# Optimization experiments

Measured on AMD Instinct MI355X. Metric: run time of the kernel, lower is better.

The kernel has to match this reference:

```python
import jax, jax.numpy as jnp
import numpy as np

NC = 2            # num_classes
CONF_THR = 0.7
IOU_THR = 0.2

_PI, _PJ = np.triu_indices(9, k=1)   # 36 candidate edge directions for min-area rect


def _decode_level(out, stride):
    # out: [C,h,w]; scale (x,y) channels by stride and add the pixel grid, flatten to [h*w, C]
    C, h, w = out.shape
    gw = (stride * jnp.arange(w, dtype=out.dtype))[None, :]
    gh = (stride * jnp.arange(h, dtype=out.dtype))[:, None]
    out = out.at[NC + 1].set(out[NC + 1] * stride + gw)
    out = out.at[NC + 2].set(out[NC + 2] * stride + gh)
    return out.reshape(C, -1).T


def _min_area_polygons(pts18):
    # pts18: (N,18) interleaved (a,b) coordinate pairs of 9 points.
    # Min-area enclosing rectangle: optimal rect is aligned with some point-pair direction;
    # brute-force all 36 pairs (superset of hull edges) -> exact result, fully vectorized.
    P = pts18.reshape(-1, 9, 2)                       # (N,9,2)
    d = P[:, _PJ] - P[:, _PI]                         # (N,36,2)
    nrm = jnp.sqrt(jnp.sum(d * d, -1) + 1e-12)
    c, s = d[..., 0] / nrm, d[..., 1] / nrm           # (N,36)
    a, b = P[..., 0][:, None, :], P[..., 1][:, None, :]   # (N,1,9)
    u = a * c[..., None] + b * s[..., None]           # rotate by -theta
    v = -a * s[..., None] + b * c[..., None]
    umin, umax = u.min(-1), u.max(-1)
    vmin, vmax = v.min(-1), v.max(-1)
    area = (umax - umin) * (vmax - vmin)              # (N,36)
    k = jnp.argmin(area, 1)[:, None]
    tk = lambda z: jnp.take_along_axis(z, k, 1)[:, 0]
    c, s, umin, umax, vmin, vmax = map(tk, (c, s, umin, umax, vmin, vmax))
    cu = jnp.stack([umin, umax, umax, umin], -1)      # rect corners in rotated frame
    cv = jnp.stack([vmin, vmin, vmax, vmax], -1)
    ca = cu * c[:, None] - cv * s[:, None]            # rotate back
    cb = cu * s[:, None] + cv * c[:, None]
    return jnp.stack([ca, cb], -1).reshape(-1, 8)     # (N,8) interleaved corners


def _points_in_quad(pts, quad):
    # pts (M,2), quad (4,2) convex with consistent winding -> (M,) bool
    e = jnp.roll(quad, -1, 0) - quad
    r = pts[:, None, :] - quad[None]
    cr = e[None, :, 0] * r[..., 1] - e[None, :, 1] * r[..., 0]
    return (cr >= 0).all(-1) | (cr <= 0).all(-1)


def _box_decoder(rect):
    # rect (N,8) -> (N,5) [cx, cy, w, h, angle]; y_first=True convention from the source
    w = jnp.sqrt((rect[:, 0] - rect[:, 2]) ** 2 + (rect[:, 1] - rect[:, 3]) ** 2)
    h = jnp.sqrt((rect[:, 4] - rect[:, 2]) ** 2 + (rect[:, 5] - rect[:, 3]) ** 2)
    cx = rect[:, 1:8:2].sum(1) * 0.25
    cy = rect[:, 0:8:2].sum(1) * 0.25
    ang = jnp.arctan((rect[:, 0] - rect[:, 2]) / (rect[:, 1] - rect[:, 3]))
    return jnp.stack([cx, cy, w, h, ang], -1)


def _rbox_corners(b):
    cx, cy, w, h, a = b[0], b[1], b[2], b[3], b[4]
    cs, sn = jnp.cos(a), jnp.sin(a)
    lx = jnp.array([-0.5, 0.5, 0.5, -0.5]) * w
    ly = jnp.array([-0.5, -0.5, 0.5, 0.5]) * h
    return jnp.stack([cx + lx * cs - ly * sn, cy + lx * sn + ly * cs], -1)  # (4,2)


def _quad_inter_area(A, B):
    # exact intersection area of two convex quads A,B (4,2):
    # candidates = corners of each inside the other + all 16 edge-edge intersections,
    # sorted by angle around their centroid, masked shoelace.
    inA = _points_in_quad(B, A)
    inB = _points_in_quad(A, B)
    rA = jnp.roll(A, -1, 0) - A
    rB = jnp.roll(B, -1, 0) - B
    qp = B[None] - A[:, None]                                  # (4,4,2)
    den = rA[:, None, 0] * rB[None, :, 1] - rA[:, None, 1] * rB[None, :, 0]
    dsafe = jnp.where(jnp.abs(den) < 1e-9, 1e-9, den)
    t = (qp[..., 0] * rB[None, :, 1] - qp[..., 1] * rB[None, :, 0]) / dsafe
    uu = (qp[..., 0] * rA[:, None, 1] - qp[..., 1] * rA[:, None, 0]) / dsafe
    okx = (jnp.abs(den) > 1e-9) & (t >= 0) & (t <= 1) & (uu >= 0) & (uu <= 1)
    X = A[:, None] + t[..., None] * rA[:, None]
    pts = jnp.concatenate([A, B, X.reshape(16, 2)], 0)          # (24,2)
    val = jnp.concatenate([inB, inA, okx.reshape(16)], 0)
    n = val.sum()
    cen = jnp.sum(jnp.where(val[:, None], pts, 0.0), 0) / jnp.maximum(n, 1)
    rel = pts - cen
    ang = jnp.where(val, jnp.arctan2(rel[:, 1], rel[:, 0]), 1e9)
    o = jnp.argsort(ang)
    rp, vs = rel[o], val[o]
    rp = jnp.where(vs[:, None], rp, rp[0])   # invalid slots -> first valid vertex (zero-area edges)
    nx = jnp.roll(rp, -1, 0)
    area = 0.5 * jnp.abs(jnp.sum(rp[:, 0] * nx[:, 1] - rp[:, 1] * nx[:, 0]))
    return jnp.where(n >= 3, area, 0.0)


def _forward(out3, out4, out5, off1_l3, off1_l4, off1_l5, offf_l3, offf_l4, offf_l5):
    outs = jnp.concatenate([_decode_level(out3[0], 4),
                            _decode_level(out4[0], 8),
                            _decode_level(out5[0], 16)], 0)          # (N, NC+3)
    flat = lambda z: z[0].reshape(18, -1).T
    off1 = jnp.concatenate([flat(off1_l3), flat(off1_l4), flat(off1_l5)], 0)
    offf = jnp.concatenate([flat(offf_l3), flat(offf_l4), flat(offf_l5)], 0) + off1
    N = outs.shape[0]
    x, y = outs[:, NC + 1], outs[:, NC + 2]
    offf = offf + jnp.tile(jnp.stack([y, x], -1), (1, 9))            # (y,x) interleaved, 9 points
    xs, ys = offf[:, 1:18:2], offf[:, 0:18:2]
    area = (xs.max(1) - xs.min(1)) * (ys.max(1) - ys.min(1)) / 40.0
    conf = outs[:, 0]
    conf_mask = conf > CONF_THR * jax.nn.sigmoid(area)
    rect = _min_area_polygons(offf)                                  # (N,8)
    boxes5 = _box_decoder(rect)                                      # (N,5)
    corners = jax.vmap(_rbox_corners)(boxes5)                        # (N,4,2)
    areas5 = boxes5[:, 2] * boxes5[:, 3]
    position = outs[:, NC + 1:]                                      # (N,2) = (x,y)
    pts_yx = jnp.stack([position[:, 1], position[:, 0]], -1)         # (y,x), matches rect plane
    quads = rect.reshape(N, 4, 2)
    order = jnp.argsort(jnp.where(conf_mask, conf, -jnp.inf))[::-1]

    def step(carry, i):
        suppressed, keep = carry
        active = jnp.logical_not(suppressed[i])
        keep = keep.at[i].set(active)
        inside = _points_in_quad(pts_yx, quads[i])                   # points_in_polygons
        inter = jax.vmap(lambda C: _quad_inter_area(corners[i], C))(corners)
        iou = inter / (areas5[i] + areas5 - inter + 1e-9)            # box_iou_rotated
        suppressed = suppressed | (active & (inside | (iou >= IOU_THR)))
        return (suppressed, keep), None

    init = (jnp.logical_not(conf_mask), jnp.zeros(N, dtype=bool))
    (_, keep), _ = jax.lax.scan(step, init, order)

    cls = outs[:, 1:NC + 1]
    maxc = cls.max(1)
    masks = jnp.stack([keep & (cls[:, i] == maxc) for i in range(NC)], 0)  # (NC,N)
    cnt = masks.sum(1)
    result = jnp.where(masks[:, :, None], position[None], 0.0)             # (NC,N,2) padded
    rect_out = rect * keep[:, None].astype(rect.dtype)                     # (N,8) padded
    return cnt, result, rect_out


def setup_inputs() -> dict:
    key = jax.random.key(0)
    shapes = [("out3", (1, NC + 3, 32, 32)), ("out4", (1, NC + 3, 16, 16)), ("out5", (1, NC + 3, 8, 8)),
              ("off1_l3", (1, 18, 32, 32)), ("off1_l4", (1, 18, 16, 16)), ("off1_l5", (1, 18, 8, 8)),
              ("offf_l3", (1, 18, 32, 32)), ("offf_l4", (1, 18, 16, 16)), ("offf_l5", (1, 18, 8, 8))]
    ks = jax.random.split(key, len(shapes))
    return {n: jax.random.normal(k, s, dtype=jnp.float32) for (n, s), k in zip(shapes, ks)}


def reference(out3, out4, out5, off1_l3, off1_l4, off1_l5, offf_l3, offf_l4, offf_l5):
    return _forward(out3, out4, out5, off1_l3, off1_l4, off1_l5, offf_l3, offf_l4, offf_l5)
```

## Files before the change

kernel.cpp:

```cpp
#include <hip/hip_runtime.h>
#include <math.h>

#define N_DET 1344
#define NW 21
#define MW_MAX 8
#define T2S 9
#define PAIR_CAP 40000


__device__ __forceinline__ bool pt_in_quad4(const float* qx, const float* qy,
                                            float px, float py) {
    bool allp = true, alln = true;
#pragma unroll
    for (int k = 0; k < 4; k++) {
        int k1 = (k + 1) & 3;
        float ex = qx[k1] - qx[k], ey = qy[k1] - qy[k];
        float rx = px - qx[k],     ry = py - qy[k];
        float cr = ex * ry - ey * rx;
        allp = allp && (cr >= 0.f);
        alln = alln && (cr <= 0.f);
    }
    return allp || alln;
}

__device__ float quad_inter_area(const float* Ax, const float* Ay,
                                 const float* Bx, const float* By) {
    float px[24], py[24];
    unsigned vmask = 0;
    int n = 0;
#pragma unroll
    for (int k = 0; k < 4; k++) {
        px[k] = Ax[k]; py[k] = Ay[k];
        if (pt_in_quad4(Bx, By, Ax[k], Ay[k])) { vmask |= 1u << k; n++; }
    }
#pragma unroll
    for (int k = 0; k < 4; k++) {
        px[4 + k] = Bx[k]; py[4 + k] = By[k];
        if (pt_in_quad4(Ax, Ay, Bx[k], By[k])) { vmask |= 1u << (4 + k); n++; }
    }
#pragma unroll
    for (int k = 0; k < 4; k++) {
        int k1 = (k + 1) & 3;
        float rax = Ax[k1] - Ax[k], ray = Ay[k1] - Ay[k];
#pragma unroll
        for (int l = 0; l < 4; l++) {
            int l1 = (l + 1) & 3;
            float rbx = Bx[l1] - Bx[l], rby = By[l1] - By[l];
            float qpx = Bx[l] - Ax[k],  qpy = By[l] - Ay[k];
            float den = rax * rby - ray * rbx;
            float ad  = fabsf(den);
            float dsafe = (ad < 1e-9f) ? 1e-9f : den;
            float t = (qpx * rby - qpy * rbx) / dsafe;
            float u = (qpx * ray - qpy * rax) / dsafe;
            bool ok = (ad > 1e-9f) && t >= 0.f && t <= 1.f && u >= 0.f && u <= 1.f;
            int id = 8 + k * 4 + l;
            px[id] = Ax[k] + t * rax;
            py[id] = Ay[k] + t * ray;
            if (ok) { vmask |= 1u << id; n++; }
        }
    }
    float cx = 0.f, cy = 0.f;
#pragma unroll
    for (int m = 0; m < 24; m++)
        if ((vmask >> m) & 1u) { cx += px[m]; cy += py[m]; }
    int mx = (n < 1) ? 1 : n;
    cx = cx / (float)mx;
    cy = cy / (float)mx;

    unsigned long long key[32];
    float sx[32], sy[32];
#pragma unroll
    for (int m = 0; m < 24; m++) {
        float rx = px[m] - cx, ry = py[m] - cy;
        float a = ((vmask >> m) & 1u) ? atan2f(ry, rx) : 1e9f;
        unsigned u = __float_as_uint(a);
        u = (u & 0x80000000u) ? ~u : (u | 0x80000000u);
        key[m] = (((unsigned long long)u) << 6) | (unsigned)m;
        sx[m] = rx; sy[m] = ry;
    }
#pragma unroll
    for (int m = 24; m < 32; m++) { key[m] = ~0ull; sx[m] = 0.f; sy[m] = 0.f; }

#pragma unroll
    for (int k = 2; k <= 32; k <<= 1) {
#pragma unroll
        for (int j = k >> 1; j > 0; j >>= 1) {
#pragma unroll
            for (int t = 0; t < 32; t++) {
                int l = t ^ j;
                if (l > t) {
                    bool up = ((t & k) == 0);
                    bool sw = up ? (key[t] > key[l]) : (key[t] < key[l]);
                    if (sw) {
                        unsigned long long tk = key[t]; key[t] = key[l]; key[l] = tk;
                        float tx = sx[t]; sx[t] = sx[l]; sx[l] = tx;
                        float ty = sy[t]; sy[t] = sy[l]; sy[l] = ty;
                    }
                }
            }
        }
    }

    unsigned ut = __float_as_uint(1e9f) | 0x80000000u;
    unsigned long long kt = ((unsigned long long)ut) << 6;
    float fx = sx[0], fy = sy[0];
    float qx2[24], qy2[24];
#pragma unroll
    for (int m = 0; m < 24; m++) {
        bool v = key[m] < kt;
        qx2[m] = v ? sx[m] : fx;
        qy2[m] = v ? sy[m] : fy;
    }
    float ssum = 0.f;
#pragma unroll
    for (int m = 0; m < 24; m++) {
        int m1 = (m + 1) % 24;
        ssum += qx2[m] * qy2[m1] - qy2[m] * qx2[m1];
    }
    float area = 0.5f * fabsf(ssum);
    return (n >= 3) ? area : 0.f;
}

__device__ bool iou_suppress(const float* __restrict__ cor, const float* __restrict__ a5,
                             int i, int j) {
    float Axr[4], Ayr[4], Bxr[4], Byr[4];
#pragma unroll
    for (int k = 0; k < 4; k++) {
        Axr[k] = cor[i * 8 + 2 * k]; Ayr[k] = cor[i * 8 + 2 * k + 1];
        Bxr[k] = cor[j * 8 + 2 * k]; Byr[k] = cor[j * 8 + 2 * k + 1];
    }
    float inter = quad_inter_area(Axr, Ayr, Bxr, Byr);
    float iou = inter / (a5[i] + a5[j] - inter + 1e-9f);
    return iou >= 0.2f;
}

__global__ void k_decode(const float* __restrict__ out3, const float* __restrict__ out4,
                         const float* __restrict__ out5,
                         const float* __restrict__ o1l3, const float* __restrict__ o1l4,
                         const float* __restrict__ o1l5,
                         const float* __restrict__ ofl3, const float* __restrict__ ofl4,
                         const float* __restrict__ ofl5,
                         float* conf, float* cls0, float* cls1, float* xx, float* yy,
                         float* a5, float* ccx, float* ccy, float* rr,
                         float* rect, float* cor, int* mask, int* Mcnt, int* pairCnt) {
    int n = blockIdx.x * blockDim.x + threadIdx.x;
    if (n >= N_DET) return;
    if (n == 0) { *Mcnt = 0; *pairCnt = 0; }
    const float *out, *o1, *of;
    int w, idx; float stride;
    if (n < 1024)      { out = out3; o1 = o1l3; of = ofl3; w = 32; idx = n;        stride = 4.f; }
    else if (n < 1280) { out = out4; o1 = o1l4; of = ofl4; w = 16; idx = n - 1024; stride = 8.f; }
    else               { out = out5; o1 = o1l5; of = ofl5; w = 8;  idx = n - 1280; stride = 16.f; }
    int hw = w * w;
    int row = idx / w, col = idx % w;
    float cf = out[0 * hw + idx];
    float c0 = out[1 * hw + idx];
    float c1 = out[2 * hw + idx];
    float x  = out[3 * hw + idx] * stride + stride * (float)col;
    float y  = out[4 * hw + idx] * stride + stride * (float)row;

    float Pa[9], Pb[9];
    float minb = INFINITY, maxb = -INFINITY, mina = INFINITY, maxa = -INFINITY;
#pragma unroll
    for (int k = 0; k < 9; k++) {
        float a = of[(2 * k) * hw + idx]     + o1[(2 * k) * hw + idx]     + y;
        float b = of[(2 * k + 1) * hw + idx] + o1[(2 * k + 1) * hw + idx] + x;
        Pa[k] = a; Pb[k] = b;
        mina = fminf(mina, a); maxa = fmaxf(maxa, a);
        minb = fminf(minb, b); maxb = fmaxf(maxb, b);
    }
    float area = (maxb - minb) * (maxa - mina) / 40.0f;
    float sg = 1.0f / (1.0f + expf(-area));
    int m = (cf > 0.7f * sg) ? 1 : 0;

    float best = INFINITY, bc = 0.f, bs = 0.f;
    float bumin = 0.f, bumax = 0.f, bvmin = 0.f, bvmax = 0.f;
#pragma unroll
    for (int i = 0; i < 9; i++) {
#pragma unroll
        for (int j = i + 1; j < 9; j++) {
            float d0 = Pa[j] - Pa[i], d1 = Pb[j] - Pb[i];
            float nr = sqrtf(d0 * d0 + d1 * d1 + 1e-12f);
            float c = d0 / nr, s = d1 / nr;
            float umin = INFINITY, umax = -INFINITY, vmin = INFINITY, vmax = -INFINITY;
#pragma unroll
            for (int k = 0; k < 9; k++) {
                float u =  Pa[k] * c + Pb[k] * s;
                float v = -Pa[k] * s + Pb[k] * c;
                umin = fminf(umin, u); umax = fmaxf(umax, u);
                vmin = fminf(vmin, v); vmax = fmaxf(vmax, v);
            }
            float ar = (umax - umin) * (vmax - vmin);
            if (ar < best) { best = ar; bc = c; bs = s;
                             bumin = umin; bumax = umax; bvmin = vmin; bvmax = vmax; }
        }
    }
    float cu[4] = {bumin, bumax, bumax, bumin};
    float cv[4] = {bvmin, bvmin, bvmax, bvmax};
    float r8[8];
#pragma unroll
    for (int k = 0; k < 4; k++) {
        r8[2 * k]     = cu[k] * bc - cv[k] * bs;
        r8[2 * k + 1] = cu[k] * bs + cv[k] * bc;
    }
    float w5 = sqrtf((r8[0] - r8[2]) * (r8[0] - r8[2]) + (r8[1] - r8[3]) * (r8[1] - r8[3]));
    float h5 = sqrtf((r8[4] - r8[2]) * (r8[4] - r8[2]) + (r8[5] - r8[3]) * (r8[5] - r8[3]));
    float cx = (r8[1] + r8[3] + r8[5] + r8[7]) * 0.25f;
    float cy = (r8[0] + r8[2] + r8[4] + r8[6]) * 0.25f;
    float ang = atanf((r8[0] - r8[2]) / (r8[1] - r8[3]));
    float cs = cosf(ang), sn = sinf(ang);
    const float lxs[4] = {-0.5f, 0.5f, 0.5f, -0.5f};
    const float lys[4] = {-0.5f, -0.5f, 0.5f, 0.5f};
#pragma unroll
    for (int k = 0; k < 4; k++) {
        cor[n * 8 + 2 * k]     = cx + lxs[k] * w5 * cs - lys[k] * h5 * sn;
        cor[n * 8 + 2 * k + 1] = cy + lxs[k] * w5 * sn + lys[k] * h5 * cs;
    }
#pragma unroll
    for (int k = 0; k < 8; k++) rect[n * 8 + k] = r8[k];
    conf[n] = cf; cls0[n] = c0; cls1[n] = c1;
    xx[n] = x; yy[n] = y; a5[n] = w5 * h5; mask[n] = m;
    ccx[n] = cx; ccy[n] = cy;
    rr[n] = 0.5f * sqrtf(w5 * w5 + h5 * h5);
}

__global__ __launch_bounds__(64) void k_order(const float* __restrict__ conf,
                                              const int* __restrict__ mask,
                                              int* order, int* Mcnt) {
    int b = blockIdx.x;
    int lane = threadIdx.x;
    int mb = mask[b];
    float ki = mb ? conf[b] : -INFINITY;
    int rank = 0;
    for (int j = lane; j < N_DET; j += 64) {
        float kj = mask[j] ? conf[j] : -INFINITY;
        rank += ((kj > ki) || (kj == ki && j > b)) ? 1 : 0;
    }
    for (int off = 32; off; off >>= 1) rank += __shfl_down(rank, off, 64);
    if (lane == 0) {
        order[rank] = b;
        if (mb) atomicAdd(Mcnt, 1);
    }
}

__global__ __launch_bounds__(256) void k_pairs_a(
        const float* __restrict__ rect, const float* __restrict__ cor,
        const float* __restrict__ a5,
        const float* __restrict__ xx, const float* __restrict__ yy,
        const float* __restrict__ ccx, const float* __restrict__ ccy,
        const float* __restrict__ rr,
        const int* __restrict__ order, const int* __restrict__ Mcnt,
        unsigned long long* __restrict__ S2, unsigned int* __restrict__ pairs,
        int* __restrict__ pairCnt) {
    int M = *Mcnt;
    if (M <= 0) return;
    int MW = (M + 63) >> 6;
    bool use_list = (MW <= MW_MAX);
    int lane  = threadIdx.x & 63;
    int gwave = (blockIdx.x * 256 + threadIdx.x) >> 6;
    int nwave = (gridDim.x * 256) >> 6;
    int total = M * MW;
    for (int t = gwave; t < total; t += nwave) {
        int p = t / MW;
        int w = t - p * MW;
        int i = order[p];
        int q = w * 64 + lane;
        bool valid = q < M;
        int j = valid ? order[q] : i;

        float cbi = ccx[i], cai = ccy[i], ri = rr[i];
        float da = yy[j] - cai, db = xx[j] - cbi;
        float rin = ri + 0.1f;
        bool inside = false;
        if (da * da + db * db <= rin * rin) {
            float qxr[4], qyr[4];
#pragma unroll
            for (int k = 0; k < 4; k++) { qxr[k] = rect[i * 8 + 2 * k]; qyr[k] = rect[i * 8 + 2 * k + 1]; }
            inside = pt_in_quad4(qxr, qyr, yy[j], xx[j]);
        }
        bool bit = valid && inside;
        unsigned long long bb = __ballot(bit);
        if (lane == 0) S2[p * MW + w] = bb;

        float ex = cbi - ccx[j], ey = cai - ccy[j];
        float rs = ri + rr[j] + 0.1f;
        bool iou_pos = valid && (q != p) && !bit && (ex * ex + ey * ey <= rs * rs);
        if (use_list) {
            unsigned long long pm = __ballot(iou_pos);
            if (pm) {
                int cw = __popcll(pm);
                int base = 0;
                if (lane == 0) base = atomicAdd(pairCnt, cw);
                base = __shfl(base, 0, 64);
                if (iou_pos) {
                    int pos = base + __popcll(pm & ((1ull << lane) - 1ull));
                    if (pos < PAIR_CAP) {
                        pairs[pos] = ((unsigned)p << 11) | (unsigned)q;
                    } else if (iou_suppress(cor, a5, i, j)) {
                        atomicOr(&S2[p * MW + w], 1ull << (q & 63));
                    }
                }
            }
        } else if (iou_pos) {
            if (iou_suppress(cor, a5, i, j))
                atomicOr(&S2[p * MW + w], 1ull << (q & 63));
        }
    }
}

__global__ __launch_bounds__(256) void k_pairs_b(
        const float* __restrict__ cor, const float* __restrict__ a5,
        const int* __restrict__ order, const int* __restrict__ Mcnt,
        const int* __restrict__ pairCnt, const unsigned int* __restrict__ pairs,
        unsigned long long* __restrict__ S2) {
    int M = *Mcnt;
    int MW = (M + 63) >> 6;
    if (MW > MW_MAX) return;
    int cnt = *pairCnt; if (cnt > PAIR_CAP) cnt = PAIR_CAP;
    int stride = gridDim.x * 256;
    for (int t = blockIdx.x * 256 + threadIdx.x; t < cnt; t += stride) {
        unsigned v = pairs[t];
        int p = (int)(v >> 11), q = (int)(v & 2047u);
        int i = order[p], j = order[q];
        if (iou_suppress(cor, a5, i, j))
            atomicOr(&S2[p * MW + (q >> 6)], 1ull << (q & 63));
    }
}

__global__ __launch_bounds__(512) void k_scan_out(
    const float* __restrict__ cls0, const float* __restrict__ cls1,
    const float* __restrict__ xx, const float* __restrict__ yy,
    const float* __restrict__ rect,
    const int* __restrict__ order, const int* __restrict__ Mcnt,
    const unsigned long long* __restrict__ S2, float* __restrict__ out) {
    __shared__ int order_s[N_DET];
    __shared__ unsigned long long T2[512 * T2S];
    __shared__ unsigned long long Kfin[MW_MAX];
    __shared__ unsigned int keep32[(N_DET + 31) / 32];
    __shared__ int cnt_s[2];
    int tid = threadIdx.x;
    int lane = tid & 63, wid = tid >> 6;
    int M = *Mcnt;
    int MW = (M + 63) >> 6;
    for (int t = tid; t < N_DET; t += 512) order_s[t] = order[t];
    for (int t = tid; t < (N_DET + 31) / 32; t += 512) keep32[t] = 0u;
    if (tid < 2) cnt_s[tid] = 0;
    if (tid < MW_MAX) Kfin[tid] = 0ull;
    __syncthreads();

    if (M > 0 && MW <= MW_MAX) {
        for (int blk = wid; blk < MW * MW; blk += 8) {
            int wp = blk / MW, wq = blk - wp * MW;
            int pp = wp * 64 + lane;
            unsigned long long x = (pp < M) ? S2[pp * MW + wq] : 0ull;
#pragma unroll
            for (int b = 0; b < 64; b++) {
                unsigned long long bb = __ballot((x >> b) & 1ull);
                if (lane == b) T2[(wq * 64 + b) * T2S + wp] = bb;
            }
        }
        __syncthreads();

        if (wid == 0) {
            unsigned long long kw[MW_MAX];
#pragma unroll
            for (int w = 0; w < MW_MAX; w++) {
                int lo = w * 64;
                kw[w] = (M > lo) ? ((M - lo >= 64) ? ~0ull : ((1ull << (M - lo)) - 1ull)) : 0ull;
            }
            unsigned long long pmask = lane ? ((1ull << lane) - 1ull) : 0ull;
            for (int it = 0; it <= M; ++it) {
                bool changed = false;
#pragma unroll
                for (int k = 0; k < MW_MAX; k++) {
                    if (k < MW) {
                        int q = k * 64 + lane;
                        const unsigned long long* row = &T2[q * T2S];
                        unsigned long long sup = 0ull;
#pragma unroll
                        for (int w = 0; w < MW_MAX; w++) {
                            if (w < k)       sup |= row[w] & kw[w];
                            else if (w == k) sup |= row[w] & kw[w] & pmask;
                        }
                        bool nb = (q < M) && (sup == 0ull);
                        unsigned long long nw = __ballot(nb);
                        changed |= (nw != kw[k]);
                        kw[k] = nw;
                    }
                }
                if (!changed) break;
            }
            if (lane == 0) {
#pragma unroll
                for (int w = 0; w < MW_MAX; w++) Kfin[w] = kw[w];
            }
        }
        __syncthreads();
        for (int t = tid; t < M; t += 512) {
            if ((Kfin[t >> 6] >> (t & 63)) & 1ull) {
                int i = order_s[t];
                atomicOr(&keep32[i >> 5], 1u << (i & 31));
            }
        }
    } else if (M > 0) {
        if (wid == 0) {
            unsigned long long rem = 0ull;
            int lo = lane * 64;
            if (M > lo) rem = (M - lo >= 64) ? ~0ull : ((1ull << (M - lo)) - 1ull);
            for (int guard = 0; guard < N_DET; guard++) {
                unsigned long long vote = __ballot(rem != 0ull);
                if (!vote) break;
                int w = __builtin_ctzll(vote);
                unsigned long long wd = __shfl(rem, w, 64);
                int b = __builtin_ctzll(wd);
                int p = w * 64 + b;
                int i = order_s[p];
                if (lane == 0) atomicOr(&keep32[i >> 5], 1u << (i & 31));
                unsigned long long rowv = (lane < MW) ? S2[p * MW + lane] : 0ull;
                rem &= ~rowv;
                if (lane == w) rem &= ~(1ull << b);
            }
        }
    }
    __syncthreads();

    int c0 = 0, c1 = 0;
    for (int n = tid; n < N_DET; n += 512) {
        bool kp = (keep32[n >> 5] >> (n & 31)) & 1u;
        float a = cls0[n], b = cls1[n];
        float mxc = fmaxf(a, b);
        bool m0 = kp && (a == mxc);
        bool m1 = kp && (b == mxc);
        float x = xx[n], y = yy[n];
        out[2 + 0 * N_DET * 2 + n * 2 + 0] = m0 ? x : 0.f;
        out[2 + 0 * N_DET * 2 + n * 2 + 1] = m0 ? y : 0.f;
        out[2 + 1 * N_DET * 2 + n * 2 + 0] = m1 ? x : 0.f;
        out[2 + 1 * N_DET * 2 + n * 2 + 1] = m1 ? y : 0.f;
        float kf = kp ? 1.f : 0.f;
#pragma unroll
        for (int k = 0; k < 8; k++)
            out[2 + 2 * N_DET * 2 + n * 8 + k] = rect[n * 8 + k] * kf;
        c0 += m0 ? 1 : 0;
        c1 += m1 ? 1 : 0;
    }
    if (c0) atomicAdd(&cnt_s[0], c0);
    if (c1) atomicAdd(&cnt_s[1], c1);
    __syncthreads();
    if (tid == 0) { out[0] = (float)cnt_s[0]; out[1] = (float)cnt_s[1]; }
}

extern "C" void kernel_launch(void* const* d_in, const int* in_sizes, int n_in,
                              void* d_out, int out_size, void* d_ws, size_t ws_size,
                              hipStream_t stream) {
    const float* out3 = (const float*)d_in[0];
    const float* out4 = (const float*)d_in[1];
    const float* out5 = (const float*)d_in[2];
    const float* o1l3 = (const float*)d_in[3];
    const float* o1l4 = (const float*)d_in[4];
    const float* o1l5 = (const float*)d_in[5];
    const float* ofl3 = (const float*)d_in[6];
    const float* ofl4 = (const float*)d_in[7];
    const float* ofl5 = (const float*)d_in[8];
    float* out = (float*)d_out;

    const int N = N_DET;
    float* wsf  = (float*)d_ws;
    float* conf = wsf + 0 * N;
    float* cls0 = wsf + 1 * N;
    float* cls1 = wsf + 2 * N;
    float* xx   = wsf + 3 * N;
    float* yy   = wsf + 4 * N;
    float* a5   = wsf + 5 * N;
    float* ccx  = wsf + 6 * N;
    float* ccy  = wsf + 7 * N;
    float* rr   = wsf + 8 * N;
    float* rect = wsf + 9 * N;
    float* cor  = wsf + 17 * N;
    int* mask   = (int*)(wsf + 25 * N);
    int* order  = mask + N;
    int* Mcnt   = order + N;
    int* pairCnt = Mcnt + 1;
    unsigned long long* S2 = (unsigned long long*)(wsf + 27 * N + 4);
    unsigned int* pairs = (unsigned int*)((char*)S2 + 32768);

    k_decode<<<(N + 255) / 256, 256, 0, stream>>>(out3, out4, out5, o1l3, o1l4, o1l5,
                                                  ofl3, ofl4, ofl5,
                                                  conf, cls0, cls1, xx, yy, a5,
                                                  ccx, ccy, rr, rect, cor, mask, Mcnt, pairCnt);
    k_order<<<N, 64, 0, stream>>>(conf, mask, order, Mcnt);
    k_pairs_a<<<1024, 256, 0, stream>>>(rect, cor, a5, xx, yy, ccx, ccy, rr,
                                        order, Mcnt, S2, pairs, pairCnt);
    k_pairs_b<<<64, 256, 0, stream>>>(cor, a5, order, Mcnt, pairCnt, pairs, S2);
    k_scan_out<<<1, 512, 0, stream>>>(cls0, cls1, xx, yy, rect, order, Mcnt, S2, out);
}
```

Baseline: 142.9 us.

## Fuse NMS pipeline into single cooperative kernel with grid-wide syncs

Replaces five separate kernel launches (decode, ordering, pair test, pair IoU, scan/output) with one cooperative kernel of 256 blocks that uses grid.sync between phases. The mask count moves from an atomic to per-wave ballot counts, and the bitmask transpose is spread across the grid instead of running in one block. This targets launch and inter-kernel gaps in a latency-bound pipeline, at the cost of grid barriers and fewer waves for the ordering and pair phases. The pair-list capacity is also raised.

```diff
diff --git a/kernel.cpp b/kernel.cpp
--- a/kernel.cpp
+++ b/kernel.cpp
@@ -1,11 +1,13 @@
 #include <hip/hip_runtime.h>
+#include <hip/hip_cooperative_groups.h>
 #include <math.h>
 
 #define N_DET 1344
-#define NW 21
 #define MW_MAX 8
 #define T2S 9
-#define PAIR_CAP 40000
+#define PAIR_CAP 200000
+
+namespace cg = cooperative_groups;
 
 
 __device__ __forceinline__ bool pt_in_quad4(const float* qx, const float* qy,
@@ -134,234 +136,220 @@
     return iou >= 0.2f;
 }
 
-__global__ void k_decode(const float* __restrict__ out3, const float* __restrict__ out4,
-                         const float* __restrict__ out5,
-                         const float* __restrict__ o1l3, const float* __restrict__ o1l4,
-                         const float* __restrict__ o1l5,
-                         const float* __restrict__ ofl3, const float* __restrict__ ofl4,
-                         const float* __restrict__ ofl5,
-                         float* conf, float* cls0, float* cls1, float* xx, float* yy,
-                         float* a5, float* ccx, float* ccy, float* rr,
-                         float* rect, float* cor, int* mask, int* Mcnt, int* pairCnt) {
-    int n = blockIdx.x * blockDim.x + threadIdx.x;
-    if (n >= N_DET) return;
-    if (n == 0) { *Mcnt = 0; *pairCnt = 0; }
-    const float *out, *o1, *of;
-    int w, idx; float stride;
-    if (n < 1024)      { out = out3; o1 = o1l3; of = ofl3; w = 32; idx = n;        stride = 4.f; }
-    else if (n < 1280) { out = out4; o1 = o1l4; of = ofl4; w = 16; idx = n - 1024; stride = 8.f; }
-    else               { out = out5; o1 = o1l5; of = ofl5; w = 8;  idx = n - 1280; stride = 16.f; }
-    int hw = w * w;
-    int row = idx / w, col = idx % w;
-    float cf = out[0 * hw + idx];
-    float c0 = out[1 * hw + idx];
-    float c1 = out[2 * hw + idx];
-    float x  = out[3 * hw + idx] * stride + stride * (float)col;
-    float y  = out[4 * hw + idx] * stride + stride * (float)row;
-
-    float Pa[9], Pb[9];
-    float minb = INFINITY, maxb = -INFINITY, mina = INFINITY, maxa = -INFINITY;
-#pragma unroll
-    for (int k = 0; k < 9; k++) {
-        float a = of[(2 * k) * hw + idx]     + o1[(2 * k) * hw + idx]     + y;
-        float b = of[(2 * k + 1) * hw + idx] + o1[(2 * k + 1) * hw + idx] + x;
-        Pa[k] = a; Pb[k] = b;
-        mina = fminf(mina, a); maxa = fmaxf(maxa, a);
-        minb = fminf(minb, b); maxb = fmaxf(maxb, b);
-    }
-    float area = (maxb - minb) * (maxa - mina) / 40.0f;
-    float sg = 1.0f / (1.0f + expf(-area));
-    int m = (cf > 0.7f * sg) ? 1 : 0;
-
-    float best = INFINITY, bc = 0.f, bs = 0.f;
-    float bumin = 0.f, bumax = 0.f, bvmin = 0.f, bvmax = 0.f;
-#pragma unroll
-    for (int i = 0; i < 9; i++) {
-#pragma unroll
-        for (int j = i + 1; j < 9; j++) {
-            float d0 = Pa[j] - Pa[i], d1 = Pb[j] - Pb[i];
-            float nr = sqrtf(d0 * d0 + d1 * d1 + 1e-12f);
-            float c = d0 / nr, s = d1 / nr;
-            float umin = INFINITY, umax = -INFINITY, vmin = INFINITY, vmax = -INFINITY;
-#pragma unroll
-            for (int k = 0; k < 9; k++) {
-                float u =  Pa[k] * c + Pb[k] * s;
-                float v = -Pa[k] * s + Pb[k] * c;
-                umin = fminf(umin, u); umax = fmaxf(umax, u);
-                vmin = fminf(vmin, v); vmax = fmaxf(vmax, v);
-            }
-            float ar = (umax - umin) * (vmax - vmin);
-            if (ar < best) { best = ar; bc = c; bs = s;
-                             bumin = umin; bumax = umax; bvmin = vmin; bvmax = vmax; }
-        }
-    }
-    float cu[4] = {bumin, bumax, bumax, bumin};
-    float cv[4] = {bvmin, bvmin, bvmax, bvmax};
-    float r8[8];
-#pragma unroll
-    for (int k = 0; k < 4; k++) {
-        r8[2 * k]     = cu[k] * bc - cv[k] * bs;
-        r8[2 * k + 1] = cu[k] * bs + cv[k] * bc;
-    }
-    float w5 = sqrtf((r8[0] - r8[2]) * (r8[0] - r8[2]) + (r8[1] - r8[3]) * (r8[1] - r8[3]));
-    float h5 = sqrtf((r8[4] - r8[2]) * (r8[4] - r8[2]) + (r8[5] - r8[3]) * (r8[5] - r8[3]));
-    float cx = (r8[1] + r8[3] + r8[5] + r8[7]) * 0.25f;
-    float cy = (r8[0] + r8[2] + r8[4] + r8[6]) * 0.25f;
-    float ang = atanf((r8[0] - r8[2]) / (r8[1] - r8[3]));
-    float cs = cosf(ang), sn = sinf(ang);
-    const float lxs[4] = {-0.5f, 0.5f, 0.5f, -0.5f};
-    const float lys[4] = {-0.5f, -0.5f, 0.5f, 0.5f};
-#pragma unroll
-    for (int k = 0; k < 4; k++) {
-        cor[n * 8 + 2 * k]     = cx + lxs[k] * w5 * cs - lys[k] * h5 * sn;
-        cor[n * 8 + 2 * k + 1] = cy + lxs[k] * w5 * sn + lys[k] * h5 * cs;
-    }
-#pragma unroll
-    for (int k = 0; k < 8; k++) rect[n * 8 + k] = r8[k];
-    conf[n] = cf; cls0[n] = c0; cls1[n] = c1;
-    xx[n] = x; yy[n] = y; a5[n] = w5 * h5; mask[n] = m;
-    ccx[n] = cx; ccy[n] = cy;
-    rr[n] = 0.5f * sqrtf(w5 * w5 + h5 * h5);
-}
-
-__global__ __launch_bounds__(64) void k_order(const float* __restrict__ conf,
-                                              const int* __restrict__ mask,
-                                              int* order, int* Mcnt) {
-    int b = blockIdx.x;
-    int lane = threadIdx.x;
-    int mb = mask[b];
-    float ki = mb ? conf[b] : -INFINITY;
-    int rank = 0;
-    for (int j = lane; j < N_DET; j += 64) {
-        float kj = mask[j] ? conf[j] : -INFINITY;
-        rank += ((kj > ki) || (kj == ki && j > b)) ? 1 : 0;
-    }
-    for (int off = 32; off; off >>= 1) rank += __shfl_down(rank, off, 64);
-    if (lane == 0) {
-        order[rank] = b;
-        if (mb) atomicAdd(Mcnt, 1);
-    }
-}
-
-__global__ __launch_bounds__(256) void k_pairs_a(
-        const float* __restrict__ rect, const float* __restrict__ cor,
-        const float* __restrict__ a5,
-        const float* __restrict__ xx, const float* __restrict__ yy,
-        const float* __restrict__ ccx, const float* __restrict__ ccy,
-        const float* __restrict__ rr,
-        const int* __restrict__ order, const int* __restrict__ Mcnt,
-        unsigned long long* __restrict__ S2, unsigned int* __restrict__ pairs,
-        int* __restrict__ pairCnt) {
-    int M = *Mcnt;
-    if (M <= 0) return;
+struct KArgs {
+    const float *out3, *out4, *out5, *o1l3, *o1l4, *o1l5, *ofl3, *ofl4, *ofl5;
+    float *keyArr, *cls0, *cls1, *xx, *yy, *a5, *ccx, *ccy, *rr, *rect, *cor;
+    int *order, *mcount_w, *pairCnt;
+    unsigned long long *S2, *T2g;
+    unsigned int *pairs;
+    float *out;
+};
+
+__global__ __launch_bounds__(256) void k_all(KArgs a) {
+    cg::grid_group grid = cg::this_grid();
+    const int tid  = threadIdx.x;
+    const int bid  = blockIdx.x;
+    const int lane = tid & 63;
+    const int wib  = tid >> 6;
+    const int gwave = bid * 4 + wib;
+
+    if (bid < 21 && wib == 0) {
+        int n = bid * 64 + lane;
+        const float *out, *o1, *of;
+        int w, idx; float stride;
+        if (n < 1024)      { out = a.out3; o1 = a.o1l3; of = a.ofl3; w = 32; idx = n;        stride = 4.f; }
+        else if (n < 1280) { out = a.out4; o1 = a.o1l4; of = a.ofl4; w = 16; idx = n - 1024; stride = 8.f; }
+        else               { out = a.out5; o1 = a.o1l5; of = a.ofl5; w = 8;  idx = n - 1280; stride = 16.f; }
+        int hw = w * w;
+        int row = idx / w, col = idx % w;
+        float cf = out[0 * hw + idx];
+        float c0 = out[1 * hw + idx];
+        float c1 = out[2 * hw + idx];
+        float x  = out[3 * hw + idx] * stride + stride * (float)col;
+        float y  = out[4 * hw + idx] * stride + stride * (float)row;
+
+        float Pa[9], Pb[9];
+        float minb = INFINITY, maxb = -INFINITY, mina = INFINITY, maxa = -INFINITY;
+#pragma unroll
+        for (int k = 0; k < 9; k++) {
+            float aa = of[(2 * k) * hw + idx]     + o1[(2 * k) * hw + idx]     + y;
+            float bb = of[(2 * k + 1) * hw + idx] + o1[(2 * k + 1) * hw + idx] + x;
+            Pa[k] = aa; Pb[k] = bb;
+            mina = fminf(mina, aa); maxa = fmaxf(maxa, aa);
+            minb = fminf(minb, bb); maxb = fmaxf(maxb, bb);
+        }
+        float area = (maxb - minb) * (maxa - mina) / 40.0f;
+        float sg = 1.0f / (1.0f + expf(-area));
+        int m = (cf > 0.7f * sg) ? 1 : 0;
+
+        float best = INFINITY, bc = 0.f, bs = 0.f;
+        float bumin = 0.f, bumax = 0.f, bvmin = 0.f, bvmax = 0.f;
+#pragma unroll
+        for (int i = 0; i < 9; i++) {
+#pragma unroll
+            for (int j = i + 1; j < 9; j++) {
+                float d0 = Pa[j] - Pa[i], d1 = Pb[j] - Pb[i];
+                float nr = sqrtf(d0 * d0 + d1 * d1 + 1e-12f);
+                float c = d0 / nr, s = d1 / nr;
+                float umin = INFINITY, umax = -INFINITY, vmin = INFINITY, vmax = -INFINITY;
+#pragma unroll
+                for (int k = 0; k < 9; k++) {
+                    float u =  Pa[k] * c + Pb[k] * s;
+                    float v = -Pa[k] * s + Pb[k] * c;
+                    umin = fminf(umin, u); umax = fmaxf(umax, u);
+                    vmin = fminf(vmin, v); vmax = fmaxf(vmax, v);
+                }
+                float ar = (umax - umin) * (vmax - vmin);
+                if (ar < best) { best = ar; bc = c; bs = s;
+                                 bumin = umin; bumax = umax; bvmin = vmin; bvmax = vmax; }
+            }
+        }
+        float cu[4] = {bumin, bumax, bumax, bumin};
+        float cv[4] = {bvmin, bvmin, bvmax, bvmax};
+        float r8[8];
+#pragma unroll
+        for (int k = 0; k < 4; k++) {
+            r8[2 * k]     = cu[k] * bc - cv[k] * bs;
+            r8[2 * k + 1] = cu[k] * bs + cv[k] * bc;
+        }
+        float w5 = sqrtf((r8[0] - r8[2]) * (r8[0] - r8[2]) + (r8[1] - r8[3]) * (r8[1] - r8[3]));
+        float h5 = sqrtf((r8[4] - r8[2]) * (r8[4] - r8[2]) + (r8[5] - r8[3]) * (r8[5] - r8[3]));
+        float cx = (r8[1] + r8[3] + r8[5] + r8[7]) * 0.25f;
+        float cy = (r8[0] + r8[2] + r8[4] + r8[6]) * 0.25f;
+        float ang = atanf((r8[0] - r8[2]) / (r8[1] - r8[3]));
+        float cs = cosf(ang), sn = sinf(ang);
+        const float lxs[4] = {-0.5f, 0.5f, 0.5f, -0.5f};
+        const float lys[4] = {-0.5f, -0.5f, 0.5f, 0.5f};
+#pragma unroll
+        for (int k = 0; k < 4; k++) {
+            a.cor[n * 8 + 2 * k]     = cx + lxs[k] * w5 * cs - lys[k] * h5 * sn;
+            a.cor[n * 8 + 2 * k + 1] = cy + lxs[k] * w5 * sn + lys[k] * h5 * cs;
+        }
+#pragma unroll
+        for (int k = 0; k < 8; k++) a.rect[n * 8 + k] = r8[k];
+        a.keyArr[n] = m ? cf : -INFINITY;
+        a.cls0[n] = c0; a.cls1[n] = c1;
+        a.xx[n] = x; a.yy[n] = y; a.a5[n] = w5 * h5;
+        a.ccx[n] = cx; a.ccy[n] = cy;
+        a.rr[n] = 0.5f * sqrtf(w5 * w5 + h5 * h5);
+        unsigned long long mb = __ballot(m != 0);
+        if (lane == 0) a.mcount_w[bid] = (int)__popcll(mb);
+    }
+    if (bid == 21 && tid == 0) *a.pairCnt = 0;
+    grid.sync();
+
+    int M = 0;
+#pragma unroll
+    for (int k = 0; k < 21; k++) M += a.mcount_w[k];
     int MW = (M + 63) >> 6;
-    bool use_list = (MW <= MW_MAX);
-    int lane  = threadIdx.x & 63;
-    int gwave = (blockIdx.x * 256 + threadIdx.x) >> 6;
-    int nwave = (gridDim.x * 256) >> 6;
-    int total = M * MW;
-    for (int t = gwave; t < total; t += nwave) {
-        int p = t / MW;
-        int w = t - p * MW;
-        int i = order[p];
-        int q = w * 64 + lane;
-        bool valid = q < M;
-        int j = valid ? order[q] : i;
-
-        float cbi = ccx[i], cai = ccy[i], ri = rr[i];
-        float da = yy[j] - cai, db = xx[j] - cbi;
-        float rin = ri + 0.1f;
-        bool inside = false;
-        if (da * da + db * db <= rin * rin) {
-            float qxr[4], qyr[4];
-#pragma unroll
-            for (int k = 0; k < 4; k++) { qxr[k] = rect[i * 8 + 2 * k]; qyr[k] = rect[i * 8 + 2 * k + 1]; }
-            inside = pt_in_quad4(qxr, qyr, yy[j], xx[j]);
-        }
-        bool bit = valid && inside;
-        unsigned long long bb = __ballot(bit);
-        if (lane == 0) S2[p * MW + w] = bb;
-
-        float ex = cbi - ccx[j], ey = cai - ccy[j];
-        float rs = ri + rr[j] + 0.1f;
-        bool iou_pos = valid && (q != p) && !bit && (ex * ex + ey * ey <= rs * rs);
-        if (use_list) {
-            unsigned long long pm = __ballot(iou_pos);
-            if (pm) {
-                int cw = __popcll(pm);
-                int base = 0;
-                if (lane == 0) base = atomicAdd(pairCnt, cw);
-                base = __shfl(base, 0, 64);
-                if (iou_pos) {
-                    int pos = base + __popcll(pm & ((1ull << lane) - 1ull));
-                    if (pos < PAIR_CAP) {
-                        pairs[pos] = ((unsigned)p << 11) | (unsigned)q;
-                    } else if (iou_suppress(cor, a5, i, j)) {
-                        atomicOr(&S2[p * MW + w], 1ull << (q & 63));
+    bool fast = (MW <= MW_MAX);
+
+    for (int c = gwave; c < N_DET; c += 1024) {
+        float ki = a.keyArr[c];
+        int rank = 0;
+        for (int j = lane; j < N_DET; j += 64) {
+            float kj = a.keyArr[j];
+            rank += ((kj > ki) || (kj == ki && j > c)) ? 1 : 0;
+        }
+        for (int off = 32; off; off >>= 1) rank += __shfl_down(rank, off, 64);
+        if (lane == 0) a.order[rank] = c;
+    }
+    grid.sync();
+
+    if (M > 0) {
+        int total = M * MW;
+        for (int t = gwave; t < total; t += 1024) {
+            int p = t / MW;
+            int w = t - p * MW;
+            int i = a.order[p];
+            int q = w * 64 + lane;
+            bool valid = q < M;
+            int j = valid ? a.order[q] : i;
+
+            float cbi = a.ccx[i], cai = a.ccy[i], ri = a.rr[i];
+            float da = a.yy[j] - cai, db = a.xx[j] - cbi;
+            float rin = ri + 0.1f;
+            bool inside = false;
+            if (da * da + db * db <= rin * rin) {
+                float qxr[4], qyr[4];
+#pragma unroll
+                for (int k = 0; k < 4; k++) { qxr[k] = a.rect[i * 8 + 2 * k]; qyr[k] = a.rect[i * 8 + 2 * k + 1]; }
+                inside = pt_in_quad4(qxr, qyr, a.yy[j], a.xx[j]);
+            }
+            bool bit = valid && inside;
+            unsigned long long bb = __ballot(bit);
+            if (lane == 0) a.S2[p * MW + w] = bb;
+
+            float ex = cbi - a.ccx[j], ey = cai - a.ccy[j];
+            float rs = ri + a.rr[j] + 0.1f;
+            bool iou_pos = valid && (q != p) && !bit && (ex * ex + ey * ey <= rs * rs);
+            if (fast) {
+                unsigned long long pm = __ballot(iou_pos);
+                if (pm) {
+                    int cw = __popcll(pm);
+                    int base = 0;
+                    if (lane == 0) base = atomicAdd(a.pairCnt, cw);
+                    base = __shfl(base, 0, 64);
+                    if (iou_pos) {
+                        int pos = base + __popcll(pm & ((1ull << lane) - 1ull));
+                        if (pos < PAIR_CAP) {
+                            a.pairs[pos] = ((unsigned)p << 11) | (unsigned)q;
+                        } else if (iou_suppress(a.cor, a.a5, i, j)) {
+                            atomicOr(&a.S2[p * MW + w], 1ull << (q & 63));
+                        }
                     }
                 }
-            }
-        } else if (iou_pos) {
-            if (iou_suppress(cor, a5, i, j))
-                atomicOr(&S2[p * MW + w], 1ull << (q & 63));
-        }
-    }
-}
-
-__global__ __launch_bounds__(256) void k_pairs_b(
-        const float* __restrict__ cor, const float* __restrict__ a5,
-        const int* __restrict__ order, const int* __restrict__ Mcnt,
-        const int* __restrict__ pairCnt, const unsigned int* __restrict__ pairs,
-        unsigned long long* __restrict__ S2) {
-    int M = *Mcnt;
-    int MW = (M + 63) >> 6;
-    if (MW > MW_MAX) return;
-    int cnt = *pairCnt; if (cnt > PAIR_CAP) cnt = PAIR_CAP;
-    int stride = gridDim.x * 256;
-    for (int t = blockIdx.x * 256 + threadIdx.x; t < cnt; t += stride) {
-        unsigned v = pairs[t];
-        int p = (int)(v >> 11), q = (int)(v & 2047u);
-        int i = order[p], j = order[q];
-        if (iou_suppress(cor, a5, i, j))
-            atomicOr(&S2[p * MW + (q >> 6)], 1ull << (q & 63));
-    }
-}
-
-__global__ __launch_bounds__(512) void k_scan_out(
-    const float* __restrict__ cls0, const float* __restrict__ cls1,
-    const float* __restrict__ xx, const float* __restrict__ yy,
-    const float* __restrict__ rect,
-    const int* __restrict__ order, const int* __restrict__ Mcnt,
-    const unsigned long long* __restrict__ S2, float* __restrict__ out) {
-    __shared__ int order_s[N_DET];
-    __shared__ unsigned long long T2[512 * T2S];
+            } else if (iou_pos) {
+                if (iou_suppress(a.cor, a.a5, i, j))
+                    atomicOr(&a.S2[p * MW + w], 1ull << (q & 63));
+            }
+        }
+    }
+    grid.sync();
+
+    if (M > 0 && fast) {
+        int cnt = *a.pairCnt; if (cnt > PAIR_CAP) cnt = PAIR_CAP;
+        for (int t = bid * 256 + tid; t < cnt; t += 256 * 256) {
+            unsigned v = a.pairs[t];
+            int p = (int)(v >> 11), q = (int)(v & 2047u);
+            int i = a.order[p], j = a.order[q];
+            if (iou_suppress(a.cor, a.a5, i, j))
+                atomicOr(&a.S2[p * MW + (q >> 6)], 1ull << (q & 63));
+        }
+    }
+    grid.sync();
+
+    if (M > 0 && fast && gwave < MW * MW) {
+        int wp = gwave / MW, wq = gwave - wp * MW;
+        int pp = wp * 64 + lane;
+        unsigned long long x = (pp < M) ? a.S2[pp * MW + wq] : 0ull;
+#pragma unroll
+        for (int b = 0; b < 64; b++) {
+            unsigned long long bb = __ballot((x >> b) & 1ull);
+            if (lane == b) a.T2g[(wq * 64 + b) * MW_MAX + wp] = bb;
+        }
+    }
+    grid.sync();
+
+    if (bid != 0) return;
+
+    __shared__ unsigned long long T2s[512 * T2S];
     __shared__ unsigned long long Kfin[MW_MAX];
     __shared__ unsigned int keep32[(N_DET + 31) / 32];
     __shared__ int cnt_s[2];
-    int tid = threadIdx.x;
-    int lane = tid & 63, wid = tid >> 6;
-    int M = *Mcnt;
-    int MW = (M + 63) >> 6;
-    for (int t = tid; t < N_DET; t += 512) order_s[t] = order[t];
-    for (int t = tid; t < (N_DET + 31) / 32; t += 512) keep32[t] = 0u;
+    for (int t = tid; t < (N_DET + 31) / 32; t += 256) keep32[t] = 0u;
     if (tid < 2) cnt_s[tid] = 0;
     if (tid < MW_MAX) Kfin[tid] = 0ull;
+    if (M > 0 && fast) {
+        for (int t = tid; t < MW * 64 * MW_MAX; t += 256) {
+            int q = t >> 3, w = t & 7;
+            if (w < MW) T2s[q * T2S + w] = a.T2g[t];
+        }
+    }
     __syncthreads();
 
-    if (M > 0 && MW <= MW_MAX) {
-        for (int blk = wid; blk < MW * MW; blk += 8) {
-            int wp = blk / MW, wq = blk - wp * MW;
-            int pp = wp * 64 + lane;
-            unsigned long long x = (pp < M) ? S2[pp * MW + wq] : 0ull;
-#pragma unroll
-            for (int b = 0; b < 64; b++) {
-                unsigned long long bb = __ballot((x >> b) & 1ull);
-                if (lane == b) T2[(wq * 64 + b) * T2S + wp] = bb;
-            }
-        }
-        __syncthreads();
-
-        if (wid == 0) {
+    if (M > 0 && fast) {
+        if (wib == 0) {
             unsigned long long kw[MW_MAX];
 #pragma unroll
             for (int w = 0; w < MW_MAX; w++) {
@@ -375,7 +363,7 @@
                 for (int k = 0; k < MW_MAX; k++) {
                     if (k < MW) {
                         int q = k * 64 + lane;
-                        const unsigned long long* row = &T2[q * T2S];
+                        const unsigned long long* row = &T2s[q * T2S];
                         unsigned long long sup = 0ull;
 #pragma unroll
                         for (int w = 0; w < MW_MAX; w++) {
@@ -396,14 +384,14 @@
             }
         }
         __syncthreads();
-        for (int t = tid; t < M; t += 512) {
+        for (int t = tid; t < M; t += 256) {
             if ((Kfin[t >> 6] >> (t & 63)) & 1ull) {
-                int i = order_s[t];
+                int i = a.order[t];
                 atomicOr(&keep32[i >> 5], 1u << (i & 31));
             }
         }
     } else if (M > 0) {
-        if (wid == 0) {
+        if (wib == 0) {
             unsigned long long rem = 0ull;
             int lo = lane * 64;
             if (M > lo) rem = (M - lo >= 64) ? ~0ull : ((1ull << (M - lo)) - 1ull);
@@ -414,9 +402,9 @@
                 unsigned long long wd = __shfl(rem, w, 64);
                 int b = __builtin_ctzll(wd);
                 int p = w * 64 + b;
-                int i = order_s[p];
+                int i = a.order[p];
                 if (lane == 0) atomicOr(&keep32[i >> 5], 1u << (i & 31));
-                unsigned long long rowv = (lane < MW) ? S2[p * MW + lane] : 0ull;
+                unsigned long long rowv = (lane < MW) ? a.S2[p * MW + lane] : 0ull;
                 rem &= ~rowv;
                 if (lane == w) rem &= ~(1ull << b);
             }
@@ -425,71 +413,67 @@
     __syncthreads();
 
     int c0 = 0, c1 = 0;
-    for (int n = tid; n < N_DET; n += 512) {
+    for (int n = tid; n < N_DET; n += 256) {
         bool kp = (keep32[n >> 5] >> (n & 31)) & 1u;
-        float a = cls0[n], b = cls1[n];
-        float mxc = fmaxf(a, b);
-        bool m0 = kp && (a == mxc);
-        bool m1 = kp && (b == mxc);
-        float x = xx[n], y = yy[n];
-        out[2 + 0 * N_DET * 2 + n * 2 + 0] = m0 ? x : 0.f;
-        out[2 + 0 * N_DET * 2 + n * 2 + 1] = m0 ? y : 0.f;
-        out[2 + 1 * N_DET * 2 + n * 2 + 0] = m1 ? x : 0.f;
-        out[2 + 1 * N_DET * 2 + n * 2 + 1] = m1 ? y : 0.f;
+        float av = a.cls0[n], bv = a.cls1[n];
+        float mxc = fmaxf(av, bv);
+        bool m0 = kp && (av == mxc);
+        bool m1 = kp && (bv == mxc);
+        float x = a.xx[n], y = a.yy[n];
+        a.out[2 + 0 * N_DET * 2 + n * 2 + 0] = m0 ? x : 0.f;
+        a.out[2 + 0 * N_DET * 2 + n * 2 + 1] = m0 ? y : 0.f;
+        a.out[2 + 1 * N_DET * 2 + n * 2 + 0] = m1 ? x : 0.f;
+        a.out[2 + 1 * N_DET * 2 + n * 2 + 1] = m1 ? y : 0.f;
         float kf = kp ? 1.f : 0.f;
 #pragma unroll
         for (int k = 0; k < 8; k++)
-            out[2 + 2 * N_DET * 2 + n * 8 + k] = rect[n * 8 + k] * kf;
+            a.out[2 + 2 * N_DET * 2 + n * 8 + k] = a.rect[n * 8 + k] * kf;
         c0 += m0 ? 1 : 0;
         c1 += m1 ? 1 : 0;
     }
     if (c0) atomicAdd(&cnt_s[0], c0);
     if (c1) atomicAdd(&cnt_s[1], c1);
     __syncthreads();
-    if (tid == 0) { out[0] = (float)cnt_s[0]; out[1] = (float)cnt_s[1]; }
+    if (tid == 0) { a.out[0] = (float)cnt_s[0]; a.out[1] = (float)cnt_s[1]; }
 }
 
 extern "C" void kernel_launch(void* const* d_in, const int* in_sizes, int n_in,
                               void* d_out, int out_size, void* d_ws, size_t ws_size,
                               hipStream_t stream) {
-    const float* out3 = (const float*)d_in[0];
-    const float* out4 = (const float*)d_in[1];
-    const float* out5 = (const float*)d_in[2];
-    const float* o1l3 = (const float*)d_in[3];
-    const float* o1l4 = (const float*)d_in[4];
-    const float* o1l5 = (const float*)d_in[5];
-    const float* ofl3 = (const float*)d_in[6];
-    const float* ofl4 = (const float*)d_in[7];
-    const float* ofl5 = (const float*)d_in[8];
-    float* out = (float*)d_out;
-
     const int N = N_DET;
-    float* wsf  = (float*)d_ws;
-    float* conf = wsf + 0 * N;
-    float* cls0 = wsf + 1 * N;
-    float* cls1 = wsf + 2 * N;
-    float* xx   = wsf + 3 * N;
-    float* yy   = wsf + 4 * N;
-    float* a5   = wsf + 5 * N;
-    float* ccx  = wsf + 6 * N;
-    float* ccy  = wsf + 7 * N;
-    float* rr   = wsf + 8 * N;
-    float* rect = wsf + 9 * N;
-    float* cor  = wsf + 17 * N;
-    int* mask   = (int*)(wsf + 25 * N);
-    int* order  = mask + N;
-    int* Mcnt   = order + N;
-    int* pairCnt = Mcnt + 1;
-    unsigned long long* S2 = (unsigned long long*)(wsf + 27 * N + 4);
-    unsigned int* pairs = (unsigned int*)((char*)S2 + 32768);
-
-    k_decode<<<(N + 255) / 256, 256, 0, stream>>>(out3, out4, out5, o1l3, o1l4, o1l5,
-                                                  ofl3, ofl4, ofl5,
-                                                  conf, cls0, cls1, xx, yy, a5,
-                                                  ccx, ccy, rr, rect, cor, mask, Mcnt, pairCnt);
-    k_order<<<N, 64, 0, stream>>>(conf, mask, order, Mcnt);
-    k_pairs_a<<<1024, 256, 0, stream>>>(rect, cor, a5, xx, yy, ccx, ccy, rr,
-                                        order, Mcnt, S2, pairs, pairCnt);
-    k_pairs_b<<<64, 256, 0, stream>>>(cor, a5, order, Mcnt, pairCnt, pairs, S2);
-    k_scan_out<<<1, 512, 0, stream>>>(cls0, cls1, xx, yy, rect, order, Mcnt, S2, out);
+    float* wsf = (float*)d_ws;
+
+    KArgs a;
+    a.out3 = (const float*)d_in[0];
+    a.out4 = (const float*)d_in[1];
+    a.out5 = (const float*)d_in[2];
+    a.o1l3 = (const float*)d_in[3];
+    a.o1l4 = (const float*)d_in[4];
+    a.o1l5 = (const float*)d_in[5];
+    a.ofl3 = (const float*)d_in[6];
+    a.ofl4 = (const float*)d_in[7];
+    a.ofl5 = (const float*)d_in[8];
+
+    a.keyArr = wsf + 0 * N;
+    a.cls0   = wsf + 1 * N;
+    a.cls1   = wsf + 2 * N;
+    a.xx     = wsf + 3 * N;
+    a.yy     = wsf + 4 * N;
+    a.a5     = wsf + 5 * N;
+    a.ccx    = wsf + 6 * N;
+    a.ccy    = wsf + 7 * N;
+    a.rr     = wsf + 8 * N;
+    a.rect   = wsf + 9 * N;
+    a.cor    = wsf + 17 * N;
+    int* ip  = (int*)(wsf + 25 * N);
+    a.order    = ip;
+    a.mcount_w = ip + N;
+    a.pairCnt  = ip + N + 24;
+    a.S2  = (unsigned long long*)((char*)d_ws + 26 * N * 4 + 128);
+    a.T2g = a.S2 + N * 21;
+    a.pairs = (unsigned int*)(a.T2g + 512 * MW_MAX);
+    a.out = (float*)d_out;
+
+    void* kp[] = { (void*)&a };
+    hipLaunchCooperativeKernel((const void*)k_all, dim3(256), dim3(256), kp, 0, stream);
 }
```

Measured after the change: 270.1 us. +89.0%, slower.
